# Performance work log

Measured on AMD Instinct MI355X. Metric: run time of the kernel, lower is better.

Reference implementation:

```python
import jax, jax.numpy as jnp
import numpy as np


def _gru_scan(x, m, d, Wih, Whh, bih, bhh):
    # Returns pre-update hidden at each step (hiddens.append(hidden) BEFORE rnn_cell)
    H = Whh.shape[1]
    B = x.shape[0]
    h0 = jnp.zeros((B, H), x.dtype)
    xs = (jnp.swapaxes(x, 0, 1), jnp.swapaxes(m, 0, 1), jnp.swapaxes(d, 0, 1))  # [T,B,V]

    def step(h, inp):
        xt, mt, dt = inp
        gi = jnp.concatenate([xt, mt, dt], axis=1) @ Wih.T + bih  # [B,3H]
        gh = h @ Whh.T + bhh
        ir, iz, inn = jnp.split(gi, 3, axis=1)
        hr, hz, hn = jnp.split(gh, 3, axis=1)
        r = jax.nn.sigmoid(ir + hr)
        z = jax.nn.sigmoid(iz + hz)
        n = jnp.tanh(inn + r * hn)
        h_new = (1.0 - z) * n + z * h
        return h_new, h

    _, hs = jax.lax.scan(step, h0, xs)
    return jnp.swapaxes(hs, 0, 1)  # [B,T,H]


def setup_inputs() -> dict:
    key = jax.random.key(0)
    B, T, V, H = 512, 128, 59, 512
    ks = jax.random.split(key, 12)

    def u(k, shape, fan_in):
        s = 1.0 / np.sqrt(fan_in).astype(np.float32)
        return jax.random.uniform(k, shape, jnp.float32, -s, s)

    return {
        "values": jax.random.normal(ks[0], (B, T, V), jnp.float32),
        "masks": (jax.random.uniform(ks[1], (B, T, V)) < 0.8).astype(jnp.float32),
        "deltas_f": jax.random.uniform(ks[2], (B, T, V), jnp.float32),
        "deltas_b": jax.random.uniform(ks[3], (B, T, V), jnp.float32),
        # GRUCell(input=3V, hidden=H)
        "Wih": u(ks[4], (3 * H, 3 * V), 3 * V),
        "Whh": u(ks[5], (3 * H, H), H),
        "bih": jnp.zeros((3 * H,), jnp.float32),
        "bhh": jnp.zeros((3 * H,), jnp.float32),
        # hist_reg: Linear(2H -> V)
        "Wh": u(ks[6], (V, 2 * H), 2 * H),
        "bh": jnp.zeros((V,), jnp.float32),
        "Wf": u(ks[7], (V, V), V),
        "bf": jnp.zeros((V,), jnp.float32),
        # weight_combine: Linear(2V -> V)
        "Wc": u(ks[8], (V, 2 * V), 2 * V),
        "bc": jnp.zeros((V,), jnp.float32),
        # imputation: Linear(V -> V)
        "Wi": u(ks[9], (V, V), V),
        "bi": jnp.zeros((V,), jnp.float32),
    }


def reference(values, masks, deltas_f, deltas_b, Wih, Whh, bih, bhh,
              Wh, bh, Wf, bf, Wc, bc, Wi, bi):
    V = values.shape[-1]
    # forward-direction hiddens
    hf = _gru_scan(values, masks, deltas_f, Wih, Whh, bih, bhh)  # [B,T,H]
    # backward-direction: run GRU on time-flipped x/masks with deltas_b, then reverse list
    hb = _gru_scan(values[:, ::-1], masks[:, ::-1], deltas_b, Wih, Whh, bih, bhh)[:, ::-1]
    h = jnp.concatenate([hf, hb], axis=-1)  # [B,T,2H]
    x_v = h @ Wh.T + bh  # hist_reg
    mdiag = 1.0 - jnp.eye(V, dtype=values.dtype)
    x_u = values @ (Wf * mdiag).T + bf  # feat_reg
    x_h = x_u + jnp.concatenate([x_v, masks], axis=-1) @ Wc.T + bc
    imp = x_h @ Wi.T + bi
    # per-timestep masked MAE, summed over T (denominator is per-step mask count)
    num = jnp.sum(jnp.abs(values - imp) * masks, axis=(0, 2))  # [T]
    den = jnp.sum(masks, axis=(0, 2)) + 1e-5
    x_loss = jnp.sum(num / den)
    x_imp = masks * values + (1.0 - masks) * imp
    return x_imp, x_loss
```

## Files before the change

### kernel.cpp

```cpp
#include <hip/hip_runtime.h>
#include <stdint.h>


typedef unsigned short ushort_t;
typedef __bf16 bf16x8 __attribute__((ext_vector_type(8)));
typedef float f32x4 __attribute__((ext_vector_type(4)));
typedef unsigned int u32x4 __attribute__((ext_vector_type(4)));

__device__ __forceinline__ ushort_t f2bf(float f) {
    union { float f; uint32_t u; } c; c.f = f;
    uint32_t u = c.u;
    uint32_t r = (u + 0x7FFFu + ((u >> 16) & 1u)) >> 16;
    return (ushort_t)r;
}

__device__ __forceinline__ u32x4 load_b128_cached(const void* p) {
    u32x4 d;
    asm volatile("global_load_dwordx4 %0, %1, off" : "=v"(d) : "v"(p) : "memory");
    return d;
}
__device__ __forceinline__ u32x4 load_b128_mall(const void* p) {
    u32x4 d;
    asm volatile("global_load_dwordx4 %0, %1, off sc0 sc1" : "=v"(d) : "v"(p) : "memory");
    return d;
}
__device__ __forceinline__ void store_b16_mall(void* p, unsigned v) {
    asm volatile("global_store_short %0, %1, off sc0 sc1" :: "v"(p), "v"(v) : "memory");
}

__device__ __forceinline__ float fast_sigmoid(float x) {
    float e = __expf(-x);
    return __builtin_amdgcn_rcpf(1.f + e);
}
__device__ __forceinline__ float fast_tanh(float x) {
    float xc = fminf(fmaxf(x, -15.f), 15.f);
    float e = __expf(-2.f * xc);
    return (1.f - e) * __builtin_amdgcn_rcpf(1.f + e);
}

__global__ void prep_small(const float* __restrict__ Wih, const float* __restrict__ Whh,
                           const float* __restrict__ Wh,
                           const float* __restrict__ Wf, const float* __restrict__ bf_,
                           const float* __restrict__ Wc, const float* __restrict__ bc,
                           const float* __restrict__ Wi, const float* __restrict__ bi,
                           ushort_t* __restrict__ WhhB, ushort_t* __restrict__ WihB,
                           ushort_t* __restrict__ WhpB,
                           ushort_t* __restrict__ hf0, ushort_t* __restrict__ hb0,
                           float* __restrict__ hstate,
                           ushort_t* __restrict__ Wpost1, ushort_t* __restrict__ Wpost2,
                           float* __restrict__ bcP, float* __restrict__ biP,
                           unsigned* __restrict__ bar, float* __restrict__ outp)
{
    long long gid = (long long)blockIdx.x * blockDim.x + threadIdx.x;
    long long stride = (long long)gridDim.x * blockDim.x;

    if (gid == 0) outp[3866624] = 0.f;
    for (long long i = gid; i < 16 * 64; i += stride) bar[i] = 0u;
    for (long long i = gid; i < 1024LL * 512; i += stride) hstate[i] = 0.f;
    for (long long i = gid; i < 512LL * 512; i += stride) { hf0[i] = 0; hb0[i] = 0; }
    for (long long i = gid; i < 1536LL * 512; i += stride) WhhB[i] = f2bf(Whh[i]);
    for (long long i = gid; i < 1536LL * 192; i += stride) {
        int n = (int)(i / 192), c = (int)(i % 192);
        WihB[i] = (c < 177) ? f2bf(Wih[n * 177 + c]) : (ushort_t)0;
    }
    for (long long i = gid; i < 64LL * 1024; i += stride) {
        int n = (int)(i >> 10), k = (int)(i & 1023);
        WhpB[i] = (n < 59) ? f2bf(Wh[n * 1024 + k]) : (ushort_t)0;
    }
    for (long long i = gid; i < 64LL * 192; i += stride) {
        int n = (int)(i / 192), c = (int)(i % 192);
        float w = 0.f;
        if (n < 59) {
            if (c < 59)       w = (c == n) ? 0.f : Wf[n * 59 + c];
            else if (c < 118) w = Wc[n * 118 + (c - 59)];
            else if (c < 177) w = Wc[n * 118 + 59 + (c - 118)];
        }
        Wpost1[i] = f2bf(w);
    }
    for (long long i = gid; i < 64LL * 64; i += stride) {
        int n = (int)(i >> 6), k = (int)(i & 63);
        Wpost2[i] = (n < 59 && k < 59) ? f2bf(Wi[n * 59 + k]) : (ushort_t)0;
    }
    for (long long i = gid; i < 64; i += stride) {
        bcP[i] = (i < 59) ? (bf_[i] + bc[i]) : 0.f;
        biP[i] = (i < 59) ? bi[i] : 0.f;
    }
}

__global__ __launch_bounds__(192)
void prep_panels(const float* __restrict__ values, const float* __restrict__ masks,
                 const float* __restrict__ deltas_f, const float* __restrict__ deltas_b,
                 ushort_t* __restrict__ xcat_f, ushort_t* __restrict__ xcat_b,
                 ushort_t* __restrict__ pcat)
{
    const int row = blockIdx.x;
    const int c = threadIdx.x;
    const int b = row >> 7, t = row & 127;
    const int tr = 127 - t;
    const long long rowr = (long long)b * 128 + tr;

    float vf = 0.f;
    if (c < 59)       vf = values  [(long long)row * 59 + c];
    else if (c < 118) vf = masks   [(long long)row * 59 + (c - 59)];
    else if (c < 177) vf = deltas_f[(long long)row * 59 + (c - 118)];
    xcat_f[((size_t)t * 512 + b) * 192 + c] = (c < 177) ? f2bf(vf) : (ushort_t)0;

    float vb = 0.f;
    if (c < 59)       vb = values  [rowr * 59 + c];
    else if (c < 118) vb = masks   [rowr * 59 + (c - 59)];
    else if (c < 177) vb = deltas_b[(long long)row * 59 + (c - 118)];
    xcat_b[((size_t)t * 512 + b) * 192 + c] = (c < 177) ? f2bf(vb) : (ushort_t)0;

    if (c < 59)
        pcat[(size_t)row * 192 + c] = f2bf(values[(long long)row * 59 + c]);
    else if (c >= 118 && c < 177)
        pcat[(size_t)row * 192 + c] = f2bf(masks[(long long)row * 59 + (c - 118)]);
    else if (c >= 177)
        pcat[(size_t)row * 192 + c] = 0;
}

__global__ __launch_bounds__(512)
void recurrence_kernel(const ushort_t* __restrict__ WhhB, const ushort_t* __restrict__ WihB,
                       const float* __restrict__ bih, const float* __restrict__ bhh,
                       const ushort_t* __restrict__ xcat_f, const ushort_t* __restrict__ xcat_b,
                       ushort_t* __restrict__ hfS, ushort_t* __restrict__ hbS,
                       unsigned* __restrict__ bar)
{
    extern __shared__ char smem_c[];
    ushort_t* Bw = (ushort_t*)smem_c;
    ushort_t* As = Bw + 96 * 704;

    const int tid  = threadIdx.x;
    const int blk  = blockIdx.x;
    const int ublk = blk & 15;
    const int mblk = blk >> 4;
    const int u0   = ublk * 32;
    const bool fwd = (mblk < 8);
    const int rbase = (fwd ? mblk : mblk - 8) * 64;
    const ushort_t* xbase = fwd ? xcat_f : xcat_b;
    ushort_t* hS = fwd ? hfS : hbS;
    unsigned* gctr = bar + (unsigned)mblk * 64;

    for (int i = tid; i < 96 * 88; i += 512) {
        int row = i / 88, q = i - row * 88;
        int g = row >> 5, u = u0 + (row & 31);
        const ushort_t* src = (q < 64)
            ? WhhB + ((size_t)(g * 512 + u)) * 512 + q * 8
            : WihB + ((size_t)(g * 512 + u)) * 192 + (q - 64) * 8;
        int qs = q ^ (row & 7);
        *(u32x4*)&Bw[row * 704 + qs * 8] = *(const u32x4*)src;
    }

    const int lane = tid & 63, wv = tid >> 6;
    const int mt = wv >> 1, tc = wv & 1;
    const int l15 = lane & 15, lhi = lane >> 4;
    const int arow = tid >> 3, aj = tid & 7;
    const int awoff = arow * 64 + ((aj ^ (arow & 7)) * 8);
    const int aSw = l15 & 7;

    const int u = u0 + tc * 16 + l15;
    const float bR  = bih[u] + bhh[u];
    const float bZ  = bih[512 + u] + bhh[512 + u];
    const float bNX = bih[1024 + u];
    const float bNH = bhh[1024 + u];
    asm volatile("" :: "v"(bR), "v"(bZ), "v"(bNX), "v"(bNH));
    asm volatile("s_waitcnt vmcnt(0) lgkmcnt(0)" ::: "memory");
    __syncthreads();

    f32x4 hreg = {0.f, 0.f, 0.f, 0.f};
    f32x4 zero = {0.f, 0.f, 0.f, 0.f};
    u32x4 rx[3];
    u32x4 rh[5];

    auto mfma_pos = [&](int cbuf, int jBbase, f32x4& aR, f32x4& aZ, f32x4& accN) {
        const ushort_t* Ab = As + cbuf * 4096;
        #pragma unroll
        for (int ks = 0; ks < 64; ks += 32) {
            int j  = (ks >> 3) + lhi;
            int jB = jBbase + j;
            bf16x8 a  = *(const bf16x8*)&Ab[(mt * 16 + l15) * 64 + ((j ^ aSw) * 8)];
            bf16x8 b0 = *(const bf16x8*)&Bw[( 0 + tc * 16 + l15) * 704 + ((jB ^ aSw) * 8)];
            bf16x8 b1 = *(const bf16x8*)&Bw[(32 + tc * 16 + l15) * 704 + ((jB ^ aSw) * 8)];
            bf16x8 b2 = *(const bf16x8*)&Bw[(64 + tc * 16 + l15) * 704 + ((jB ^ aSw) * 8)];
            aR   = __builtin_amdgcn_mfma_f32_16x16x32_bf16(a, b0, aR, 0, 0, 0);
            aZ   = __builtin_amdgcn_mfma_f32_16x16x32_bf16(a, b1, aZ, 0, 0, 0);
            accN = __builtin_amdgcn_mfma_f32_16x16x32_bf16(a, b2, accN, 0, 0, 0);
        }
    };

    {
        const ushort_t* xr0 = xbase + (size_t)(rbase + arow) * 192 + aj * 8;
        rx[0] = load_b128_cached(xr0);
        rx[1] = load_b128_cached(xr0 + 64);
        rx[2] = load_b128_cached(xr0 + 128);
    }
    asm volatile("s_waitcnt vmcnt(0)" ::: "memory");

    for (int t = 0; t < 127; ++t) {
        const ushort_t* hrow = hS + (size_t)t * 262144 + (size_t)(rbase + arow) * 512 + aj * 8;
        ushort_t* hdst = hS + (size_t)(t + 1) * 262144;

        f32x4 accR = zero, accZ = zero, accNX = zero, accNH = zero;

        rh[0] = load_b128_mall(hrow);
        rh[1] = load_b128_mall(hrow + 64);
        rh[2] = load_b128_mall(hrow + 128);

        *(u32x4*)&As[awoff] = rx[0];
        __syncthreads();

        mfma_pos(0, 64, accR, accZ, accNX);
        rh[3] = load_b128_mall(hrow + 3 * 64);
        *(u32x4*)&As[4096 + awoff] = rx[1];
        __syncthreads();

        mfma_pos(1, 72, accR, accZ, accNX);
        rh[4] = load_b128_mall(hrow + 4 * 64);
        *(u32x4*)&As[awoff] = rx[2];
        {
            const ushort_t* xrn = xbase + (size_t)(t + 1) * 98304
                                + (size_t)(rbase + arow) * 192 + aj * 8;
            rx[0] = load_b128_cached(xrn);
            rx[1] = load_b128_cached(xrn + 64);
            rx[2] = load_b128_cached(xrn + 128);
        }
        __syncthreads();

        mfma_pos(0, 80, accR, accZ, accNX);
        asm volatile("s_waitcnt vmcnt(7)" ::: "memory");
        *(u32x4*)&As[4096 + awoff] = rh[0];
        rh[0] = load_b128_mall(hrow + 5 * 64);
        __syncthreads();

        mfma_pos(1, 0, accR, accZ, accNH);
        asm volatile("s_waitcnt vmcnt(7)" ::: "memory");
        *(u32x4*)&As[awoff] = rh[1];
        rh[1] = load_b128_mall(hrow + 6 * 64);
        __syncthreads();

        mfma_pos(0, 8, accR, accZ, accNH);
        asm volatile("s_waitcnt vmcnt(7)" ::: "memory");
        *(u32x4*)&As[4096 + awoff] = rh[2];
        rh[2] = load_b128_mall(hrow + 7 * 64);
        __syncthreads();

        mfma_pos(1, 16, accR, accZ, accNH);
        asm volatile("s_waitcnt vmcnt(7)" ::: "memory");
        *(u32x4*)&As[awoff] = rh[3];
        __syncthreads();

        mfma_pos(0, 24, accR, accZ, accNH);
        asm volatile("s_waitcnt vmcnt(6)" ::: "memory");
        *(u32x4*)&As[4096 + awoff] = rh[4];
        __syncthreads();

        mfma_pos(1, 32, accR, accZ, accNH);
        asm volatile("s_waitcnt vmcnt(2)" ::: "memory");
        *(u32x4*)&As[awoff] = rh[0];
        __syncthreads();

        mfma_pos(0, 40, accR, accZ, accNH);
        asm volatile("s_waitcnt vmcnt(1)" ::: "memory");
        *(u32x4*)&As[4096 + awoff] = rh[1];
        __syncthreads();

        mfma_pos(1, 48, accR, accZ, accNH);
        asm volatile("s_waitcnt vmcnt(0)" ::: "memory");
        *(u32x4*)&As[awoff] = rh[2];
        __syncthreads();

        mfma_pos(0, 56, accR, accZ, accNH);

        #pragma unroll
        for (int reg = 0; reg < 4; ++reg) {
            int m = rbase + mt * 16 + lhi * 4 + reg;
            float rr = fast_sigmoid(accR[reg] + bR);
            float zz = fast_sigmoid(accZ[reg] + bZ);
            float nn = fast_tanh(accNX[reg] + bNX + rr * (accNH[reg] + bNH));
            float hnew = (1.f - zz) * nn + zz * hreg[reg];
            hreg[reg] = hnew;
            store_b16_mall(hdst + (size_t)m * 512 + u, (unsigned)f2bf(hnew));
        }

        if (t < 126) {
            asm volatile("s_waitcnt vmcnt(0)" ::: "memory");
            __syncthreads();
            if (tid == 0) {
                atomicAdd(gctr, 1u);
                unsigned target = (unsigned)(t + 1) * 16u;
                while (__hip_atomic_load(gctr, __ATOMIC_RELAXED,
                                         __HIP_MEMORY_SCOPE_AGENT) < target)
                    __builtin_amdgcn_s_sleep(1);
            }
            __syncthreads();
        }
    }
}

__global__ __launch_bounds__(512)
void step_kernel(const ushort_t* __restrict__ hsrcF, const ushort_t* __restrict__ hsrcB,
                 ushort_t* __restrict__ hdstF, ushort_t* __restrict__ hdstB,
                 const ushort_t* __restrict__ xF, const ushort_t* __restrict__ xB,
                 const ushort_t* __restrict__ WhhB, const ushort_t* __restrict__ WihB,
                 const float* __restrict__ bih, const float* __restrict__ bhh,
                 float* __restrict__ hstate)
{
    __shared__ __align__(16) ushort_t As[64 * 64];
    __shared__ __align__(16) ushort_t Bs[96 * 64];

    const int tid  = threadIdx.x;
    const int ublk = blockIdx.x;
    const int mblk = blockIdx.y;
    const int u0   = ublk * 32;
    const bool fwd = (mblk < 8);
    const ushort_t* hsrc = fwd ? hsrcF : hsrcB;
    const ushort_t* xsrc = fwd ? xF : xB;
    ushort_t* hdst = fwd ? hdstF : hdstB;
    const int rbase = (fwd ? mblk : mblk - 8) * 64;

    const int lane = tid & 63, wv = tid >> 6;
    const int mt = wv >> 1, tc = wv & 1;
    const int l15 = lane & 15, lhi = lane >> 4;

    f32x4 zero = {0.f, 0.f, 0.f, 0.f};
    f32x4 accR = zero, accZ = zero, accNH = zero, accNX = zero;
    const int arow = tid >> 3, ac8 = (tid & 7) * 8;

    for (int chunk = 0; chunk < 11; ++chunk) {
        const bool ph1 = (chunk < 8);
        {
            const ushort_t* src = ph1
                ? hsrc + ((size_t)(rbase + arow)) * 512 + chunk * 64 + ac8
                : xsrc + ((size_t)(rbase + arow)) * 192 + (chunk - 8) * 64 + ac8;
            *(uint4*)&As[arow * 64 + ac8] = *(const uint4*)src;
        }
        {
            int rowB = tid >> 3; int c8 = (tid & 7) * 8;
            int g = rowB >> 5; int u = u0 + (rowB & 31);
            const ushort_t* src = ph1
                ? WhhB + ((size_t)(g * 512 + u)) * 512 + chunk * 64 + c8
                : WihB + ((size_t)(g * 512 + u)) * 192 + (chunk - 8) * 64 + c8;
            *(uint4*)&Bs[rowB * 64 + c8] = *(const uint4*)src;
            if (tid < 256) {
                int u2 = tid + 512;
                rowB = u2 >> 3; c8 = (u2 & 7) * 8;
                g = rowB >> 5; u = u0 + (rowB & 31);
                src = ph1
                    ? WhhB + ((size_t)(g * 512 + u)) * 512 + chunk * 64 + c8
                    : WihB + ((size_t)(g * 512 + u)) * 192 + (chunk - 8) * 64 + c8;
                *(uint4*)&Bs[rowB * 64 + c8] = *(const uint4*)src;
            }
        }
        __syncthreads();
        #pragma unroll
        for (int ks = 0; ks < 64; ks += 32) {
            bf16x8 a  = *(const bf16x8*)&As[(mt * 16 + l15) * 64 + ks + lhi * 8];
            bf16x8 b0 = *(const bf16x8*)&Bs[( 0 + tc * 16 + l15) * 64 + ks + lhi * 8];
            bf16x8 b1 = *(const bf16x8*)&Bs[(32 + tc * 16 + l15) * 64 + ks + lhi * 8];
            bf16x8 b2 = *(const bf16x8*)&Bs[(64 + tc * 16 + l15) * 64 + ks + lhi * 8];
            accR = __builtin_amdgcn_mfma_f32_16x16x32_bf16(a, b0, accR, 0, 0, 0);
            accZ = __builtin_amdgcn_mfma_f32_16x16x32_bf16(a, b1, accZ, 0, 0, 0);
            if (ph1) accNH = __builtin_amdgcn_mfma_f32_16x16x32_bf16(a, b2, accNH, 0, 0, 0);
            else     accNX = __builtin_amdgcn_mfma_f32_16x16x32_bf16(a, b2, accNX, 0, 0, 0);
        }
        __syncthreads();
    }

    const int u = u0 + tc * 16 + l15;
    const float bR  = bih[u] + bhh[u];
    const float bZ  = bih[512 + u] + bhh[512 + u];
    const float bNX = bih[1024 + u];
    const float bNH = bhh[1024 + u];
    #pragma unroll
    for (int reg = 0; reg < 4; ++reg) {
        int m = mblk * 64 + mt * 16 + lhi * 4 + reg;
        float r = 1.f / (1.f + __expf(-(accR[reg] + bR)));
        float z = 1.f / (1.f + __expf(-(accZ[reg] + bZ)));
        float n = tanhf(accNX[reg] + bNX + r * (accNH[reg] + bNH));
        size_t idx = (size_t)m * 512 + u;
        float hold = hstate[idx];
        float hnew = (1.f - z) * n + z * hold;
        hstate[idx] = hnew;
        size_t bloc = (size_t)(fwd ? m : m - 512) * 512 + u;
        hdst[bloc] = f2bf(hnew);
    }
}

__global__ __launch_bounds__(256)
void xv_kernel(const ushort_t* __restrict__ hf, const ushort_t* __restrict__ hb,
               const ushort_t* __restrict__ WhpB, const float* __restrict__ bh,
               ushort_t* __restrict__ pcat)
{
    __shared__ __align__(16) ushort_t As[128 * 64];
    __shared__ __align__(16) ushort_t Bs[64 * 64];
    const int b = blockIdx.x;
    const int tid = threadIdx.x;
    const int lane = tid & 63, wv = tid >> 6;
    const int l15 = lane & 15, lhi = lane >> 4;

    f32x4 zero = {0.f, 0.f, 0.f, 0.f};
    f32x4 acc[2][4];
    #pragma unroll
    for (int i = 0; i < 2; ++i)
        #pragma unroll
        for (int j = 0; j < 4; ++j) acc[i][j] = zero;

    for (int chunk = 0; chunk < 16; ++chunk) {
        const bool fw = (chunk < 8);
        #pragma unroll
        for (int s = 0; s < 4; ++s) {
            int unit = tid + s * 256;
            int row = unit >> 3;
            int c8 = (unit & 7) * 8;
            const ushort_t* src = fw
                ? hf + ((size_t)row * 512 + b) * 512 + chunk * 64 + c8
                : hb + ((size_t)(127 - row) * 512 + b) * 512 + (chunk - 8) * 64 + c8;
            *(uint4*)&As[row * 64 + c8] = *(const uint4*)src;
        }
        #pragma unroll
        for (int s = 0; s < 2; ++s) {
            int unit = tid + s * 256;
            int row = unit >> 3;
            int c8 = (unit & 7) * 8;
            *(uint4*)&Bs[row * 64 + c8] =
                *(const uint4*)(WhpB + (size_t)row * 1024 + chunk * 64 + c8);
        }
        __syncthreads();
        #pragma unroll
        for (int ks = 0; ks < 64; ks += 32) {
            bf16x8 bfr[4];
            #pragma unroll
            for (int nt = 0; nt < 4; ++nt)
                bfr[nt] = *(const bf16x8*)&Bs[(nt * 16 + l15) * 64 + ks + lhi * 8];
            #pragma unroll
            for (int mt2 = 0; mt2 < 2; ++mt2) {
                bf16x8 a = *(const bf16x8*)&As[(wv * 32 + mt2 * 16 + l15) * 64 + ks + lhi * 8];
                #pragma unroll
                for (int nt = 0; nt < 4; ++nt)
                    acc[mt2][nt] = __builtin_amdgcn_mfma_f32_16x16x32_bf16(a, bfr[nt], acc[mt2][nt], 0, 0, 0);
            }
        }
        __syncthreads();
    }
    #pragma unroll
    for (int mt2 = 0; mt2 < 2; ++mt2) {
        #pragma unroll
        for (int nt = 0; nt < 4; ++nt) {
            int col = nt * 16 + l15;
            if (col < 59) {
                float bhc = bh[col];
                #pragma unroll
                for (int reg = 0; reg < 4; ++reg) {
                    int t = wv * 32 + mt2 * 16 + lhi * 4 + reg;
                    pcat[((size_t)b * 128 + t) * 192 + 59 + col] = f2bf(acc[mt2][nt][reg] + bhc);
                }
            }
        }
    }
}

__global__ __launch_bounds__(256)
void post_kernel(const ushort_t* __restrict__ pcat,
                 const ushort_t* __restrict__ Wpost1, const ushort_t* __restrict__ Wpost2,
                 const float* __restrict__ bcP, const float* __restrict__ biP,
                 const float* __restrict__ values, const float* __restrict__ masks,
                 float* __restrict__ out, float* __restrict__ pnum, float* __restrict__ pden)
{
    __shared__ __align__(16) ushort_t A1[64 * 200];
    __shared__ __align__(16) ushort_t B1[64 * 200];
    __shared__ __align__(16) ushort_t B2[64 * 72];

    const int tid = threadIdx.x;
    const int blk = blockIdx.x;
    const int lane = tid & 63, wv = tid >> 6;
    const int l15 = lane & 15, lhi = lane >> 4;

    #pragma unroll
    for (int s = 0; s < 6; ++s) {
        int unit = tid + s * 256;
        int row = unit / 24, c8 = (unit % 24) * 8;
        *(uint4*)&A1[row * 200 + c8] =
            *(const uint4*)(pcat + ((size_t)blk * 64 + row) * 192 + c8);
        *(uint4*)&B1[row * 200 + c8] =
            *(const uint4*)(Wpost1 + (size_t)row * 192 + c8);
    }
    #pragma unroll
    for (int s = 0; s < 2; ++s) {
        int unit = tid + s * 256;
        int row = unit >> 3, c8 = (unit & 7) * 8;
        *(uint4*)&B2[row * 72 + c8] = *(const uint4*)(Wpost2 + (size_t)row * 64 + c8);
    }
    __syncthreads();

    f32x4 zero = {0.f, 0.f, 0.f, 0.f};
    f32x4 acc1[4];
    #pragma unroll
    for (int nt = 0; nt < 4; ++nt) acc1[nt] = zero;

    #pragma unroll
// ... 52 lines not shown
                dsum += m;
            }
        }
        #pragma unroll
        for (int o = 1; o < 16; o <<= 1) {
            esum += __shfl_xor(esum, o);
            dsum += __shfl_xor(dsum, o);
        }
        if (l15 == 0) { pnum[rowg] = esum; pden[rowg] = dsum; }
    }
}

__global__ __launch_bounds__(256)
void loss_kernel(const float* __restrict__ pnum, const float* __restrict__ pden,
                 float* __restrict__ out)
{
    __shared__ float sn[4], sd[4];
    const int t = blockIdx.x;
    const int tid = threadIdx.x;
    float a = 0.f, b = 0.f;
    for (int bb = tid; bb < 512; bb += 256) {
        a += pnum[(size_t)bb * 128 + t];
        b += pden[(size_t)bb * 128 + t];
    }
    #pragma unroll
    for (int o = 32; o >= 1; o >>= 1) {
        a += __shfl_xor(a, o);
        b += __shfl_xor(b, o);
    }
    const int wv = tid >> 6;
    if ((tid & 63) == 0) { sn[wv] = a; sd[wv] = b; }
    __syncthreads();
    if (tid == 0) {
        float A = sn[0] + sn[1] + sn[2] + sn[3];
        float B = sd[0] + sd[1] + sd[2] + sd[3];
        atomicAdd(out + 3866624, A / (B + 1e-5f));
    }
}

extern "C" void kernel_launch(void* const* d_in, const int* in_sizes, int n_in,
                              void* d_out, int out_size, void* d_ws, size_t ws_size,
                              hipStream_t stream)
{
    const float* values   = (const float*)d_in[0];
    const float* masks    = (const float*)d_in[1];
    const float* deltas_f = (const float*)d_in[2];
    const float* deltas_b = (const float*)d_in[3];
    const float* Wih = (const float*)d_in[4];
    const float* Whh = (const float*)d_in[5];
    const float* bih = (const float*)d_in[6];
    const float* bhh = (const float*)d_in[7];
    const float* Wh  = (const float*)d_in[8];
    const float* bh  = (const float*)d_in[9];
    const float* Wf  = (const float*)d_in[10];
    const float* bf_ = (const float*)d_in[11];
    const float* Wc  = (const float*)d_in[12];
    const float* bc  = (const float*)d_in[13];
    const float* Wi  = (const float*)d_in[14];
    const float* bi  = (const float*)d_in[15];
    float* out = (float*)d_out;

    uint8_t* ws = (uint8_t*)d_ws;
    size_t off = 0;
    auto alloc = [&](size_t bytes) -> void* {
        void* p = ws + off;
        off = (off + bytes + 255) & ~((size_t)255);
        return p;
    };
    ushort_t* xcat_f = (ushort_t*)alloc(128ULL * 512 * 192 * 2);
    ushort_t* xcat_b = (ushort_t*)alloc(128ULL * 512 * 192 * 2);
    ushort_t* WhhB   = (ushort_t*)alloc(1536ULL * 512 * 2);
    ushort_t* WihB   = (ushort_t*)alloc(1536ULL * 192 * 2);
    ushort_t* WhpB   = (ushort_t*)alloc(64ULL * 1024 * 2);
    ushort_t* hfS    = (ushort_t*)alloc(128ULL * 512 * 512 * 2);
    ushort_t* hbS    = (ushort_t*)alloc(128ULL * 512 * 512 * 2);
    float*    hstate = (float*)alloc(1024ULL * 512 * 4);
    ushort_t* pcat   = (ushort_t*)alloc(65536ULL * 192 * 2);
    ushort_t* Wpost1 = (ushort_t*)alloc(64ULL * 192 * 2);
    ushort_t* Wpost2 = (ushort_t*)alloc(64ULL * 64 * 2);
    float*    bcP    = (float*)alloc(64 * 4);
    float*    biP    = (float*)alloc(64 * 4);
    float*    pnum   = (float*)alloc(65536ULL * 4);
    float*    pden   = (float*)alloc(65536ULL * 4);
    unsigned* bar    = (unsigned*)alloc(16 * 64 * 4);

    prep_small<<<1024, 256, 0, stream>>>(Wih, Whh, Wh, Wf, bf_, Wc, bc, Wi, bi,
                                         WhhB, WihB, WhpB, hfS, hbS, hstate,
                                         Wpost1, Wpost2, bcP, biP, bar, out);
    prep_panels<<<65536, 192, 0, stream>>>(values, masks, deltas_f, deltas_b,
                                           xcat_f, xcat_b, pcat);

    const unsigned smemBytes = (96u * 704u + 2u * 64u * 64u) * 2u;
    hipError_t aerr = hipFuncSetAttribute((const void*)recurrence_kernel,
                                          hipFuncAttributeMaxDynamicSharedMemorySize,
                                          (int)smemBytes);
    hipError_t lerr = hipErrorUnknown;
    if (aerr == hipSuccess) {
        const ushort_t* a0 = WhhB; const ushort_t* a1 = WihB;
        const float* a2 = bih; const float* a3 = bhh;
        const ushort_t* a4 = xcat_f; const ushort_t* a5 = xcat_b;
        ushort_t* a6 = hfS; ushort_t* a7 = hbS;
        unsigned* a8 = bar;
        void* args[] = { &a0, &a1, &a2, &a3, &a4, &a5, &a6, &a7, &a8 };
        lerr = hipLaunchCooperativeKernel((const void*)recurrence_kernel,
                                          dim3(256), dim3(512), args, smemBytes, stream);
    }
    if (lerr != hipSuccess) {
        for (int t = 0; t < 127; ++t) {
            step_kernel<<<dim3(16, 16), 512, 0, stream>>>(
                hfS + (size_t)t * 512 * 512, hbS + (size_t)t * 512 * 512,
                hfS + (size_t)(t + 1) * 512 * 512, hbS + (size_t)(t + 1) * 512 * 512,
                xcat_f + (size_t)t * 512 * 192, xcat_b + (size_t)t * 512 * 192,
                WhhB, WihB, bih, bhh, hstate);
        }
    }

    xv_kernel<<<512, 256, 0, stream>>>(hfS, hbS, WhpB, bh, pcat);
    post_kernel<<<1024, 256, 0, stream>>>(pcat, Wpost1, Wpost2, bcP, biP,
                                          values, masks, out, pnum, pden);
    loss_kernel<<<128, 256, 0, stream>>>(pnum, pden, out);
}
```

Baseline: 840.4 us.

## Replace global atomic barrier with per-producer flags and slab-blocked hidden layout

The hidden-state buffer is re-laid out so that each 32-unit column block is a contiguous slab. Each block can then write its outputs with coalesced 8-byte stores staged through LDS, instead of scattered 2-byte stores. The single atomic counter barrier per row group is replaced by per-producer flag words. Consumers poll only the 8 producers whose slab they are about to read, and split that wait so the second half overlaps the input-projection MFMAs. Block-to-(row,unit) mapping is also permuted, and h loads now use L2-scoped hints, with stores written to both L2 and MALL. This risks subtle memory-ordering issues between the flag stores and the data stores, and the layout change requires matching updates in the fallback and xv kernels.

```diff
diff --git a/kernel.cpp b/kernel.cpp
--- a/kernel.cpp
+++ b/kernel.cpp
@@ -6,6 +6,7 @@
 typedef __bf16 bf16x8 __attribute__((ext_vector_type(8)));
 typedef float f32x4 __attribute__((ext_vector_type(4)));
 typedef unsigned int u32x4 __attribute__((ext_vector_type(4)));
+typedef unsigned int u32x2 __attribute__((ext_vector_type(2)));
 
 __device__ __forceinline__ ushort_t f2bf(float f) {
     union { float f; uint32_t u; } c; c.f = f;
@@ -19,13 +20,19 @@
     asm volatile("global_load_dwordx4 %0, %1, off" : "=v"(d) : "v"(p) : "memory");
     return d;
 }
-__device__ __forceinline__ u32x4 load_b128_mall(const void* p) {
+__device__ __forceinline__ u32x4 load_b128_l2(const void* p) {
     u32x4 d;
-    asm volatile("global_load_dwordx4 %0, %1, off sc0 sc1" : "=v"(d) : "v"(p) : "memory");
+    asm volatile("global_load_dwordx4 %0, %1, off sc0" : "=v"(d) : "v"(p) : "memory");
     return d;
 }
-__device__ __forceinline__ void store_b16_mall(void* p, unsigned v) {
-    asm volatile("global_store_short %0, %1, off sc0 sc1" :: "v"(p), "v"(v) : "memory");
+__device__ __forceinline__ void store_b64_l2(void* p, u32x2 v) {
+    asm volatile("global_store_dwordx2 %0, %1, off sc0" :: "v"(p), "v"(v) : "memory");
+}
+__device__ __forceinline__ void store_b64_mall(void* p, u32x2 v) {
+    asm volatile("global_store_dwordx2 %0, %1, off sc0 sc1" :: "v"(p), "v"(v) : "memory");
+}
+__device__ __forceinline__ void store_u32_mall(void* p, unsigned v) {
+    asm volatile("global_store_dword %0, %1, off sc0 sc1" :: "v"(p), "v"(v) : "memory");
 }
 
 __device__ __forceinline__ float fast_sigmoid(float x) {
@@ -132,8 +139,8 @@
 
     const int tid  = threadIdx.x;
     const int blk  = blockIdx.x;
-    const int ublk = blk & 15;
-    const int mblk = blk >> 4;
+    const int ublk = blk >> 4;
+    const int mblk = ((blk & 7) << 1) | ((blk >> 3) & 1);
     const int u0   = ublk * 32;
     const bool fwd = (mblk < 8);
     const int rbase = (fwd ? mblk : mblk - 8) * 64;
@@ -170,7 +177,7 @@
     f32x4 hreg = {0.f, 0.f, 0.f, 0.f};
     f32x4 zero = {0.f, 0.f, 0.f, 0.f};
     u32x4 rx[3];
-    u32x4 rh[5];
+    u32x4 rh[8];
 
     auto mfma_pos = [&](int cbuf, int jBbase, f32x4& aR, f32x4& aZ, f32x4& accN) {
         const ushort_t* Ab = As + cbuf * 4096;
@@ -188,6 +195,9 @@
         }
     };
 
+    const size_t hoff = (size_t)(aj >> 2) * 16384
+                      + (size_t)(rbase + arow) * 32 + (size_t)(aj & 3) * 8;
+
     {
         const ushort_t* xr0 = xbase + (size_t)(rbase + arow) * 192 + aj * 8;
         rx[0] = load_b128_cached(xr0);
@@ -197,25 +207,60 @@
     asm volatile("s_waitcnt vmcnt(0)" ::: "memory");
 
     for (int t = 0; t < 127; ++t) {
-        const ushort_t* hrow = hS + (size_t)t * 262144 + (size_t)(rbase + arow) * 512 + aj * 8;
+        const ushort_t* hslab = hS + (size_t)t * 262144;
         ushort_t* hdst = hS + (size_t)(t + 1) * 262144;
 
         f32x4 accR = zero, accZ = zero, accNX = zero, accNH = zero;
 
-        rh[0] = load_b128_mall(hrow);
-        rh[1] = load_b128_mall(hrow + 64);
-        rh[2] = load_b128_mall(hrow + 128);
+        if (t > 0) {
+            if (wv == 0) {
+                bool part = (lane < 8) && (lane != ublk);
+                const unsigned* ap = gctr + lane;
+                for (;;) {
+                    bool ok = true;
+                    if (part) {
+                        unsigned v;
+                        asm volatile("global_load_dword %0, %1, off sc0 sc1\n\t"
+                                     "s_waitcnt vmcnt(0)"
+                                     : "=v"(v) : "v"(ap) : "memory");
+                        ok = (v >= (unsigned)t);
+                    }
+                    if (__ballot(ok) == ~0ULL) break;
+                    __builtin_amdgcn_s_sleep(1);
+                }
+            }
+            __syncthreads();
+        }
+
+        rh[0] = load_b128_l2(hslab + hoff);
+        rh[1] = load_b128_l2(hslab + hoff + 32768);
+        rh[2] = load_b128_l2(hslab + hoff + 2 * 32768);
+        rh[3] = load_b128_l2(hslab + hoff + 3 * 32768);
 
         *(u32x4*)&As[awoff] = rx[0];
         __syncthreads();
 
         mfma_pos(0, 64, accR, accZ, accNX);
-        rh[3] = load_b128_mall(hrow + 3 * 64);
         *(u32x4*)&As[4096 + awoff] = rx[1];
         __syncthreads();
 
         mfma_pos(1, 72, accR, accZ, accNX);
-        rh[4] = load_b128_mall(hrow + 4 * 64);
+        if (t > 0 && wv == 0) {
+            bool part = (lane >= 8) && (lane < 16) && (lane != ublk);
+            const unsigned* ap = gctr + lane;
+            for (;;) {
+                bool ok = true;
+                if (part) {
+                    unsigned v;
+                    asm volatile("global_load_dword %0, %1, off sc0 sc1\n\t"
+                                 "s_waitcnt vmcnt(4)"
+                                 : "=v"(v) : "v"(ap) : "memory");
+                    ok = (v >= (unsigned)t);
+                }
+                if (__ballot(ok) == ~0ULL) break;
+                __builtin_amdgcn_s_sleep(1);
+            }
+        }
         *(u32x4*)&As[awoff] = rx[2];
         {
             const ushort_t* xrn = xbase + (size_t)(t + 1) * 98304
@@ -227,21 +272,22 @@
         __syncthreads();
 
         mfma_pos(0, 80, accR, accZ, accNX);
-        asm volatile("s_waitcnt vmcnt(7)" ::: "memory");
+        rh[4] = load_b128_l2(hslab + hoff + 4 * 32768);
+        rh[5] = load_b128_l2(hslab + hoff + 5 * 32768);
+        rh[6] = load_b128_l2(hslab + hoff + 6 * 32768);
+        rh[7] = load_b128_l2(hslab + hoff + 7 * 32768);
+        asm volatile("s_waitcnt vmcnt(10)" ::: "memory");
         *(u32x4*)&As[4096 + awoff] = rh[0];
-        rh[0] = load_b128_mall(hrow + 5 * 64);
         __syncthreads();
 
         mfma_pos(1, 0, accR, accZ, accNH);
-        asm volatile("s_waitcnt vmcnt(7)" ::: "memory");
+        asm volatile("s_waitcnt vmcnt(9)" ::: "memory");
         *(u32x4*)&As[awoff] = rh[1];
-        rh[1] = load_b128_mall(hrow + 6 * 64);
         __syncthreads();
 
         mfma_pos(0, 8, accR, accZ, accNH);
-        asm volatile("s_waitcnt vmcnt(7)" ::: "memory");
+        asm volatile("s_waitcnt vmcnt(8)" ::: "memory");
         *(u32x4*)&As[4096 + awoff] = rh[2];
-        rh[2] = load_b128_mall(hrow + 7 * 64);
         __syncthreads();
 
         mfma_pos(1, 16, accR, accZ, accNH);
@@ -250,50 +296,52 @@
         __syncthreads();
 
         mfma_pos(0, 24, accR, accZ, accNH);
-        asm volatile("s_waitcnt vmcnt(6)" ::: "memory");
+        asm volatile("s_waitcnt vmcnt(3)" ::: "memory");
         *(u32x4*)&As[4096 + awoff] = rh[4];
         __syncthreads();
 
         mfma_pos(1, 32, accR, accZ, accNH);
         asm volatile("s_waitcnt vmcnt(2)" ::: "memory");
-        *(u32x4*)&As[awoff] = rh[0];
+        *(u32x4*)&As[awoff] = rh[5];
         __syncthreads();
 
         mfma_pos(0, 40, accR, accZ, accNH);
         asm volatile("s_waitcnt vmcnt(1)" ::: "memory");
-        *(u32x4*)&As[4096 + awoff] = rh[1];
+        *(u32x4*)&As[4096 + awoff] = rh[6];
         __syncthreads();
 
         mfma_pos(1, 48, accR, accZ, accNH);
         asm volatile("s_waitcnt vmcnt(0)" ::: "memory");
-        *(u32x4*)&As[awoff] = rh[2];
+        *(u32x4*)&As[awoff] = rh[7];
         __syncthreads();
 
         mfma_pos(0, 56, accR, accZ, accNH);
 
         #pragma unroll
         for (int reg = 0; reg < 4; ++reg) {
-            int m = rbase + mt * 16 + lhi * 4 + reg;
+            int r64 = mt * 16 + lhi * 4 + reg;
             float rr = fast_sigmoid(accR[reg] + bR);
             float zz = fast_sigmoid(accZ[reg] + bZ);
             float nn = fast_tanh(accNX[reg] + bNX + rr * (accNH[reg] + bNH));
             float hnew = (1.f - zz) * nn + zz * hreg[reg];
             hreg[reg] = hnew;
-            store_b16_mall(hdst + (size_t)m * 512 + u, (unsigned)f2bf(hnew));
-        }
-
-        if (t < 126) {
-            asm volatile("s_waitcnt vmcnt(0)" ::: "memory");
-            __syncthreads();
-            if (tid == 0) {
-                atomicAdd(gctr, 1u);
-                unsigned target = (unsigned)(t + 1) * 16u;
-                while (__hip_atomic_load(gctr, __ATOMIC_RELAXED,
-                                         __HIP_MEMORY_SCOPE_AGENT) < target)
-                    __builtin_amdgcn_s_sleep(1);
-            }
-            __syncthreads();
-        }
+            As[4096 + r64 * 40 + (tc * 16 + l15)] = f2bf(hnew);
+        }
+        __syncthreads();
+        {
+            int r64 = tid >> 3;
+            int c4  = (tid & 7) * 4;
+            u32x2 v = *(const u32x2*)&As[4096 + r64 * 40 + c4];
+            ushort_t* dst = hdst + (size_t)ublk * 16384
+                          + (size_t)(rbase + r64) * 32 + c4;
+            store_b64_l2(dst, v);
+            store_b64_mall(dst, v);
+        }
+        asm volatile("s_waitcnt vmcnt(0)" ::: "memory");
+        __syncthreads();
+
+        if (t < 126 && tid == 0)
+            store_u32_mall(gctr + ublk, (unsigned)(t + 1));
     }
 }
 
@@ -329,9 +377,13 @@
     for (int chunk = 0; chunk < 11; ++chunk) {
         const bool ph1 = (chunk < 8);
         {
-            const ushort_t* src = ph1
-                ? hsrc + ((size_t)(rbase + arow)) * 512 + chunk * 64 + ac8
-                : xsrc + ((size_t)(rbase + arow)) * 192 + (chunk - 8) * 64 + ac8;
+            const ushort_t* src;
+            if (ph1) {
+                int p = 2 * chunk + (ac8 >> 5);
+                src = hsrc + (size_t)p * 16384 + (size_t)(rbase + arow) * 32 + (ac8 & 31);
+            } else {
+                src = xsrc + ((size_t)(rbase + arow)) * 192 + (chunk - 8) * 64 + ac8;
+            }
             *(uint4*)&As[arow * 64 + ac8] = *(const uint4*)src;
         }
         {
@@ -381,7 +433,8 @@
         float hold = hstate[idx];
         float hnew = (1.f - z) * n + z * hold;
         hstate[idx] = hnew;
-        size_t bloc = (size_t)(fwd ? m : m - 512) * 512 + u;
+        int ml = fwd ? m : m - 512;
+        size_t bloc = (size_t)(u >> 5) * 16384 + (size_t)ml * 32 + (u & 31);
         hdst[bloc] = f2bf(hnew);
     }
 }
@@ -412,9 +465,13 @@
             int unit = tid + s * 256;
             int row = unit >> 3;
             int c8 = (unit & 7) * 8;
-            const ushort_t* src = fw
-                ? hf + ((size_t)row * 512 + b) * 512 + chunk * 64 + c8
-                : hb + ((size_t)(127 - row) * 512 + b) * 512 + (chunk - 8) * 64 + c8;
+            int ch = fw ? chunk : (chunk - 8);
+            int col = ch * 64 + c8;
+            int p = col >> 5, cc = col & 31;
+            int ti = fw ? row : (127 - row);
+            const ushort_t* hbase = fw ? hf : hb;
+            const ushort_t* src = hbase + (size_t)ti * 262144
+                                + (size_t)p * 16384 + (size_t)b * 32 + cc;
             *(uint4*)&As[row * 64 + c8] = *(const uint4*)src;
         }
         #pragma unroll
```

Result: slower. 998.0 us (+18.8%).

## Replace block-wide barrier with per-wave flag polling and direct register A-fragments

Applied to the files above, without the earlier changes.

Each wave now loads its own h and x A-fragments straight from global memory into registers, so the LDS staging buffer and the many __syncthreads per timestep are gone. The per-block atomic counter barrier is replaced by per-wave slot flags: each wave publishes its step number to its own padded slot and polls the 32 slots of the waves sharing its 16-row band. The aim is to cut global synchronization latency and intra-block barriers on the serial critical path. In exchange it uses more global loads per wave and relies on the cache-scope modifiers to keep cross-block visibility correct.

```diff
diff --git a/kernel.cpp b/kernel.cpp
--- a/kernel.cpp
+++ b/kernel.cpp
@@ -19,13 +19,19 @@
     asm volatile("global_load_dwordx4 %0, %1, off" : "=v"(d) : "v"(p) : "memory");
     return d;
 }
-__device__ __forceinline__ u32x4 load_b128_mall(const void* p) {
+__device__ __forceinline__ u32x4 load_b128_l2(const void* p) {
     u32x4 d;
-    asm volatile("global_load_dwordx4 %0, %1, off sc0 sc1" : "=v"(d) : "v"(p) : "memory");
+    asm volatile("global_load_dwordx4 %0, %1, off sc0" : "=v"(d) : "v"(p) : "memory");
     return d;
+}
+__device__ __forceinline__ void store_b16_l2(void* p, unsigned v) {
+    asm volatile("global_store_short %0, %1, off sc0" :: "v"(p), "v"(v) : "memory");
 }
 __device__ __forceinline__ void store_b16_mall(void* p, unsigned v) {
     asm volatile("global_store_short %0, %1, off sc0 sc1" :: "v"(p), "v"(v) : "memory");
+}
+__device__ __forceinline__ void store_u32_mall(void* p, unsigned v) {
+    asm volatile("global_store_dword %0, %1, off sc0 sc1" :: "v"(p), "v"(v) : "memory");
 }
 
 __device__ __forceinline__ float fast_sigmoid(float x) {
@@ -55,7 +61,7 @@
     long long stride = (long long)gridDim.x * blockDim.x;
 
     if (gid == 0) outp[3866624] = 0.f;
-    for (long long i = gid; i < 16 * 64; i += stride) bar[i] = 0u;
+    for (long long i = gid; i < 2048LL * 16; i += stride) bar[i] = 0u;
     for (long long i = gid; i < 1024LL * 512; i += stride) hstate[i] = 0.f;
     for (long long i = gid; i < 512LL * 512; i += stride) { hf0[i] = 0; hb0[i] = 0; }
     for (long long i = gid; i < 1536LL * 512; i += stride) WhhB[i] = f2bf(Whh[i]);
@@ -128,7 +134,6 @@
 {
     extern __shared__ char smem_c[];
     ushort_t* Bw = (ushort_t*)smem_c;
-    ushort_t* As = Bw + 96 * 704;
 
     const int tid  = threadIdx.x;
     const int blk  = blockIdx.x;
@@ -139,7 +144,6 @@
     const int rbase = (fwd ? mblk : mblk - 8) * 64;
     const ushort_t* xbase = fwd ? xcat_f : xcat_b;
     ushort_t* hS = fwd ? hfS : hbS;
-    unsigned* gctr = bar + (unsigned)mblk * 64;
 
     for (int i = tid; i < 96 * 88; i += 512) {
         int row = i / 88, q = i - row * 88;
@@ -154,8 +158,6 @@
     const int lane = tid & 63, wv = tid >> 6;
     const int mt = wv >> 1, tc = wv & 1;
     const int l15 = lane & 15, lhi = lane >> 4;
-    const int arow = tid >> 3, aj = tid & 7;
-    const int awoff = arow * 64 + ((aj ^ (arow & 7)) * 8);
     const int aSw = l15 & 7;
 
     const int u = u0 + tc * 16 + l15;
@@ -167,134 +169,127 @@
     asm volatile("s_waitcnt vmcnt(0) lgkmcnt(0)" ::: "memory");
     __syncthreads();
 
+    const unsigned bandSlot = (unsigned)(mblk * 4 + mt) * 32u;
+    const unsigned* pollp = bar + ((size_t)bandSlot + (unsigned)lane) * 16;
+    unsigned* myslot = bar + ((size_t)bandSlot + (unsigned)(ublk * 2 + tc)) * 16;
+
     f32x4 hreg = {0.f, 0.f, 0.f, 0.f};
     f32x4 zero = {0.f, 0.f, 0.f, 0.f};
-    u32x4 rx[3];
-    u32x4 rh[5];
-
-    auto mfma_pos = [&](int cbuf, int jBbase, f32x4& aR, f32x4& aZ, f32x4& accN) {
-        const ushort_t* Ab = As + cbuf * 4096;
-        #pragma unroll
-        for (int ks = 0; ks < 64; ks += 32) {
-            int j  = (ks >> 3) + lhi;
-            int jB = jBbase + j;
-            bf16x8 a  = *(const bf16x8*)&Ab[(mt * 16 + l15) * 64 + ((j ^ aSw) * 8)];
+    f32x4 accR, accZ, accNX, accNH;
+
+    u32x4 h0a, h0b, h1a, h1b, h2a, h2b, h3a, h3b;
+    u32x4 h4a, h4b, h5a, h5b, h6a, h6b, h7a, h7b;
+    u32x4 rx0a, rx0b, rx1a, rx1b, rx2a, rx2b;
+
+    auto mfma6 = [&](u32x4 fa, u32x4 fb, int jb, f32x4& accN) {
+        bf16x8 a0 = *(bf16x8*)&fa;
+        bf16x8 a1 = *(bf16x8*)&fb;
+        {
+            int jB = jb + lhi;
             bf16x8 b0 = *(const bf16x8*)&Bw[( 0 + tc * 16 + l15) * 704 + ((jB ^ aSw) * 8)];
             bf16x8 b1 = *(const bf16x8*)&Bw[(32 + tc * 16 + l15) * 704 + ((jB ^ aSw) * 8)];
             bf16x8 b2 = *(const bf16x8*)&Bw[(64 + tc * 16 + l15) * 704 + ((jB ^ aSw) * 8)];
-            aR   = __builtin_amdgcn_mfma_f32_16x16x32_bf16(a, b0, aR, 0, 0, 0);
-            aZ   = __builtin_amdgcn_mfma_f32_16x16x32_bf16(a, b1, aZ, 0, 0, 0);
-            accN = __builtin_amdgcn_mfma_f32_16x16x32_bf16(a, b2, accN, 0, 0, 0);
+            accR = __builtin_amdgcn_mfma_f32_16x16x32_bf16(a0, b0, accR, 0, 0, 0);
+            accZ = __builtin_amdgcn_mfma_f32_16x16x32_bf16(a0, b1, accZ, 0, 0, 0);
+            accN = __builtin_amdgcn_mfma_f32_16x16x32_bf16(a0, b2, accN, 0, 0, 0);
+        }
+        {
+            int jB = jb + 4 + lhi;
+            bf16x8 b0 = *(const bf16x8*)&Bw[( 0 + tc * 16 + l15) * 704 + ((jB ^ aSw) * 8)];
+            bf16x8 b1 = *(const bf16x8*)&Bw[(32 + tc * 16 + l15) * 704 + ((jB ^ aSw) * 8)];
+            bf16x8 b2 = *(const bf16x8*)&Bw[(64 + tc * 16 + l15) * 704 + ((jB ^ aSw) * 8)];
+            accR = __builtin_amdgcn_mfma_f32_16x16x32_bf16(a1, b0, accR, 0, 0, 0);
+            accZ = __builtin_amdgcn_mfma_f32_16x16x32_bf16(a1, b1, accZ, 0, 0, 0);
+            accN = __builtin_amdgcn_mfma_f32_16x16x32_bf16(a1, b2, accN, 0, 0, 0);
         }
     };
 
+    const size_t mrow = (size_t)(rbase + mt * 16 + l15);
+
     {
-        const ushort_t* xr0 = xbase + (size_t)(rbase + arow) * 192 + aj * 8;
-        rx[0] = load_b128_cached(xr0);
-        rx[1] = load_b128_cached(xr0 + 64);
-        rx[2] = load_b128_cached(xr0 + 128);
+        const ushort_t* xr = xbase + (mrow) * 192 + lhi * 8;
+        rx0a = load_b128_cached(xr);        rx0b = load_b128_cached(xr + 32);
+        rx1a = load_b128_cached(xr + 64);   rx1b = load_b128_cached(xr + 96);
+        rx2a = load_b128_cached(xr + 128);  rx2b = load_b128_cached(xr + 160);
     }
     asm volatile("s_waitcnt vmcnt(0)" ::: "memory");
+    __builtin_amdgcn_sched_barrier(0);
+
+#define HPOS(K, WN, JB)                                                       \
+    asm volatile("s_waitcnt vmcnt(" #WN ")" ::: "memory");                    \
+    __builtin_amdgcn_sched_barrier(0);                                        \
+    mfma6(h##K##a, h##K##b, (JB), accNH);
 
     for (int t = 0; t < 127; ++t) {
-        const ushort_t* hrow = hS + (size_t)t * 262144 + (size_t)(rbase + arow) * 512 + aj * 8;
-        ushort_t* hdst = hS + (size_t)(t + 1) * 262144;
-
-        f32x4 accR = zero, accZ = zero, accNX = zero, accNH = zero;
-
-        rh[0] = load_b128_mall(hrow);
-        rh[1] = load_b128_mall(hrow + 64);
-        rh[2] = load_b128_mall(hrow + 128);
-
-        *(u32x4*)&As[awoff] = rx[0];
-        __syncthreads();
-
-        mfma_pos(0, 64, accR, accZ, accNX);
-        rh[3] = load_b128_mall(hrow + 3 * 64);
-        *(u32x4*)&As[4096 + awoff] = rx[1];
-        __syncthreads();
-
-        mfma_pos(1, 72, accR, accZ, accNX);
-        rh[4] = load_b128_mall(hrow + 4 * 64);
-        *(u32x4*)&As[awoff] = rx[2];
+        if (t > 0) {
+            const unsigned target = (unsigned)t;
+            for (;;) {
+                unsigned v = 0xFFFFFFFFu;
+                if (lane < 32) {
+                    asm volatile("global_load_dword %0, %1, off sc0 sc1"
+                                 : "=v"(v) : "v"(pollp) : "memory");
+                }
+                asm volatile("s_waitcnt vmcnt(0)" ::: "memory");
+                if (__ballot(v >= target) == ~0ULL) break;
+                __builtin_amdgcn_s_sleep(1);
+            }
+            __builtin_amdgcn_sched_barrier(0);
+        }
+
         {
-            const ushort_t* xrn = xbase + (size_t)(t + 1) * 98304
-                                + (size_t)(rbase + arow) * 192 + aj * 8;
-            rx[0] = load_b128_cached(xrn);
-            rx[1] = load_b128_cached(xrn + 64);
-            rx[2] = load_b128_cached(xrn + 128);
-        }
-        __syncthreads();
-
-        mfma_pos(0, 80, accR, accZ, accNX);
-        asm volatile("s_waitcnt vmcnt(7)" ::: "memory");
-        *(u32x4*)&As[4096 + awoff] = rh[0];
-        rh[0] = load_b128_mall(hrow + 5 * 64);
-        __syncthreads();
-
-        mfma_pos(1, 0, accR, accZ, accNH);
-        asm volatile("s_waitcnt vmcnt(7)" ::: "memory");
-        *(u32x4*)&As[awoff] = rh[1];
-        rh[1] = load_b128_mall(hrow + 6 * 64);
-        __syncthreads();
-
-        mfma_pos(0, 8, accR, accZ, accNH);
-        asm volatile("s_waitcnt vmcnt(7)" ::: "memory");
-        *(u32x4*)&As[4096 + awoff] = rh[2];
-        rh[2] = load_b128_mall(hrow + 7 * 64);
-        __syncthreads();
-
-        mfma_pos(1, 16, accR, accZ, accNH);
-        asm volatile("s_waitcnt vmcnt(7)" ::: "memory");
-        *(u32x4*)&As[awoff] = rh[3];
-        __syncthreads();
-
-        mfma_pos(0, 24, accR, accZ, accNH);
-        asm volatile("s_waitcnt vmcnt(6)" ::: "memory");
-        *(u32x4*)&As[4096 + awoff] = rh[4];
-        __syncthreads();
-
-        mfma_pos(1, 32, accR, accZ, accNH);
-        asm volatile("s_waitcnt vmcnt(2)" ::: "memory");
-        *(u32x4*)&As[awoff] = rh[0];
-        __syncthreads();
-
-        mfma_pos(0, 40, accR, accZ, accNH);
-        asm volatile("s_waitcnt vmcnt(1)" ::: "memory");
-        *(u32x4*)&As[4096 + awoff] = rh[1];
-        __syncthreads();
-
-        mfma_pos(1, 48, accR, accZ, accNH);
+            const ushort_t* hr = hS + (size_t)t * 262144 + mrow * 512 + lhi * 8;
+            h0a = load_b128_l2(hr);            h0b = load_b128_l2(hr + 32);
+            h1a = load_b128_l2(hr + 64);       h1b = load_b128_l2(hr + 96);
+            h2a = load_b128_l2(hr + 128);      h2b = load_b128_l2(hr + 160);
+            h3a = load_b128_l2(hr + 192);      h3b = load_b128_l2(hr + 224);
+            h4a = load_b128_l2(hr + 256);      h4b = load_b128_l2(hr + 288);
+            h5a = load_b128_l2(hr + 320);      h5b = load_b128_l2(hr + 352);
+            h6a = load_b128_l2(hr + 384);      h6b = load_b128_l2(hr + 416);
+            h7a = load_b128_l2(hr + 448);      h7b = load_b128_l2(hr + 480);
+        }
+
+        accR = zero; accZ = zero; accNX = zero; accNH = zero;
+        mfma6(rx0a, rx0b, 64, accNX);
+        mfma6(rx1a, rx1b, 72, accNX);
+        mfma6(rx2a, rx2b, 80, accNX);
+
+        {
+            const ushort_t* xr = xbase + ((size_t)(t + 1) * 512 + mrow) * 192 + lhi * 8;
+            rx0a = load_b128_cached(xr);        rx0b = load_b128_cached(xr + 32);
+            rx1a = load_b128_cached(xr + 64);   rx1b = load_b128_cached(xr + 96);
+            rx2a = load_b128_cached(xr + 128);  rx2b = load_b128_cached(xr + 160);
+        }
+
+        HPOS(0, 20,  0)
+        HPOS(1, 18,  8)
+        HPOS(2, 16, 16)
+        HPOS(3, 14, 24)
+        HPOS(4, 12, 32)
+        HPOS(5, 10, 40)
+        HPOS(6,  8, 48)
+        HPOS(7,  6, 56)
+
+        {
+            ushort_t* hdst = hS + (size_t)(t + 1) * 262144;
+            #pragma unroll
+            for (int reg = 0; reg < 4; ++reg) {
+                float rr = fast_sigmoid(accR[reg] + bR);
+                float zz = fast_sigmoid(accZ[reg] + bZ);
+                float nn = fast_tanh(accNX[reg] + bNX + rr * (accNH[reg] + bNH));
+                float hnew = (1.f - zz) * nn + zz * hreg[reg];
+                hreg[reg] = hnew;
+                unsigned hb16 = (unsigned)f2bf(hnew);
+                ushort_t* dst = hdst + (size_t)(rbase + mt * 16 + lhi * 4 + reg) * 512 + u;
+                store_b16_l2(dst, hb16);
+                store_b16_mall(dst, hb16);
+            }
+        }
         asm volatile("s_waitcnt vmcnt(0)" ::: "memory");
-        *(u32x4*)&As[awoff] = rh[2];
-        __syncthreads();
-
-        mfma_pos(0, 56, accR, accZ, accNH);
-
-        #pragma unroll
-        for (int reg = 0; reg < 4; ++reg) {
-            int m = rbase + mt * 16 + lhi * 4 + reg;
-            float rr = fast_sigmoid(accR[reg] + bR);
-            float zz = fast_sigmoid(accZ[reg] + bZ);
-            float nn = fast_tanh(accNX[reg] + bNX + rr * (accNH[reg] + bNH));
-            float hnew = (1.f - zz) * nn + zz * hreg[reg];
-            hreg[reg] = hnew;
-            store_b16_mall(hdst + (size_t)m * 512 + u, (unsigned)f2bf(hnew));
-        }
-
-        if (t < 126) {
-            asm volatile("s_waitcnt vmcnt(0)" ::: "memory");
-            __syncthreads();
-            if (tid == 0) {
-                atomicAdd(gctr, 1u);
-                unsigned target = (unsigned)(t + 1) * 16u;
-                while (__hip_atomic_load(gctr, __ATOMIC_RELAXED,
-                                         __HIP_MEMORY_SCOPE_AGENT) < target)
-                    __builtin_amdgcn_s_sleep(1);
-            }
-            __syncthreads();
-        }
-    }
+
+        if (lane == 0)
+            store_u32_mall(myslot, (unsigned)(t + 1));
+    }
+#undef HPOS
 }
 
 __global__ __launch_bounds__(512)
@@ -633,7 +628,7 @@
     float*    biP    = (float*)alloc(64 * 4);
     float*    pnum   = (float*)alloc(65536ULL * 4);
     float*    pden   = (float*)alloc(65536ULL * 4);
-    unsigned* bar    = (unsigned*)alloc(16 * 64 * 4);
+    unsigned* bar    = (unsigned*)alloc(2048ULL * 16 * 4);
 
     prep_small<<<1024, 256, 0, stream>>>(Wih, Whh, Wh, Wf, bf_, Wc, bc, Wi, bi,
                                          WhhB, WihB, WhpB, hfS, hbS, hstate,
@@ -641,7 +636,7 @@
     prep_panels<<<65536, 192, 0, stream>>>(values, masks, deltas_f, deltas_b,
                                            xcat_f, xcat_b, pcat);
 
-    const unsigned smemBytes = (96u * 704u + 2u * 64u * 64u) * 2u;
+    const unsigned smemBytes = 96u * 704u * 2u;
     hipError_t aerr = hipFuncSetAttribute((const void*)recurrence_kernel,
                                           hipFuncAttributeMaxDynamicSharedMemorySize,
                                           (int)smemBytes);
```

Measured after the change: 3.112 ms. +270.3%, slower.

## Store hidden state in column-slab layout and remap blocks for L2 locality

Applied to the files above, without the earlier changes.

Changes the per-timestep hidden-state buffer from row-major [B,512] to 16 column slabs of [512,32], so each block writes a contiguous slab. Block-to-tile mapping is permuted so blocks sharing a unit slice are adjacent, and h loads switch from MALL-scope to L2-scope (sc0). Each store is issued twice, once at L2 scope and once at MALL scope, to keep cross-XCD visibility. All consumers (fallback recurrence, xv_kernel) are updated to the new indexing. The duplicated store and the weaker load scope could cause coherence problems across XCDs.

```diff
diff --git a/kernel.cpp b/kernel.cpp
--- a/kernel.cpp
+++ b/kernel.cpp
@@ -19,10 +19,13 @@
     asm volatile("global_load_dwordx4 %0, %1, off" : "=v"(d) : "v"(p) : "memory");
     return d;
 }
-__device__ __forceinline__ u32x4 load_b128_mall(const void* p) {
+__device__ __forceinline__ u32x4 load_b128_l2(const void* p) {
     u32x4 d;
-    asm volatile("global_load_dwordx4 %0, %1, off sc0 sc1" : "=v"(d) : "v"(p) : "memory");
+    asm volatile("global_load_dwordx4 %0, %1, off sc0" : "=v"(d) : "v"(p) : "memory");
     return d;
+}
+__device__ __forceinline__ void store_b16_l2(void* p, unsigned v) {
+    asm volatile("global_store_short %0, %1, off sc0" :: "v"(p), "v"(v) : "memory");
 }
 __device__ __forceinline__ void store_b16_mall(void* p, unsigned v) {
     asm volatile("global_store_short %0, %1, off sc0 sc1" :: "v"(p), "v"(v) : "memory");
@@ -132,8 +135,8 @@
 
     const int tid  = threadIdx.x;
     const int blk  = blockIdx.x;
-    const int ublk = blk & 15;
-    const int mblk = blk >> 4;
+    const int ublk = blk >> 4;
+    const int mblk = ((blk & 7) << 1) | ((blk >> 3) & 1);
     const int u0   = ublk * 32;
     const bool fwd = (mblk < 8);
     const int rbase = (fwd ? mblk : mblk - 8) * 64;
@@ -159,6 +162,7 @@
     const int aSw = l15 & 7;
 
     const int u = u0 + tc * 16 + l15;
+    const int cl = tc * 16 + l15;
     const float bR  = bih[u] + bhh[u];
     const float bZ  = bih[512 + u] + bhh[512 + u];
     const float bNX = bih[1024 + u];
@@ -188,6 +192,9 @@
         }
     };
 
+    const size_t hoff = (size_t)(aj >> 2) * 16384
+                      + (size_t)(rbase + arow) * 32 + (size_t)(aj & 3) * 8;
+
     {
         const ushort_t* xr0 = xbase + (size_t)(rbase + arow) * 192 + aj * 8;
         rx[0] = load_b128_cached(xr0);
@@ -197,25 +204,25 @@
     asm volatile("s_waitcnt vmcnt(0)" ::: "memory");
 
     for (int t = 0; t < 127; ++t) {
-        const ushort_t* hrow = hS + (size_t)t * 262144 + (size_t)(rbase + arow) * 512 + aj * 8;
+        const ushort_t* hslab = hS + (size_t)t * 262144 + hoff;
         ushort_t* hdst = hS + (size_t)(t + 1) * 262144;
 
         f32x4 accR = zero, accZ = zero, accNX = zero, accNH = zero;
 
-        rh[0] = load_b128_mall(hrow);
-        rh[1] = load_b128_mall(hrow + 64);
-        rh[2] = load_b128_mall(hrow + 128);
+        rh[0] = load_b128_l2(hslab);
+        rh[1] = load_b128_l2(hslab + 32768);
+        rh[2] = load_b128_l2(hslab + 2 * 32768);
 
         *(u32x4*)&As[awoff] = rx[0];
         __syncthreads();
 
         mfma_pos(0, 64, accR, accZ, accNX);
-        rh[3] = load_b128_mall(hrow + 3 * 64);
+        rh[3] = load_b128_l2(hslab + 3 * 32768);
         *(u32x4*)&As[4096 + awoff] = rx[1];
         __syncthreads();
 
         mfma_pos(1, 72, accR, accZ, accNX);
-        rh[4] = load_b128_mall(hrow + 4 * 64);
+        rh[4] = load_b128_l2(hslab + 4 * 32768);
         *(u32x4*)&As[awoff] = rx[2];
         {
             const ushort_t* xrn = xbase + (size_t)(t + 1) * 98304
@@ -229,19 +236,19 @@
         mfma_pos(0, 80, accR, accZ, accNX);
         asm volatile("s_waitcnt vmcnt(7)" ::: "memory");
         *(u32x4*)&As[4096 + awoff] = rh[0];
-        rh[0] = load_b128_mall(hrow + 5 * 64);
+        rh[0] = load_b128_l2(hslab + 5 * 32768);
         __syncthreads();
 
         mfma_pos(1, 0, accR, accZ, accNH);
         asm volatile("s_waitcnt vmcnt(7)" ::: "memory");
         *(u32x4*)&As[awoff] = rh[1];
-        rh[1] = load_b128_mall(hrow + 6 * 64);
+        rh[1] = load_b128_l2(hslab + 6 * 32768);
         __syncthreads();
 
         mfma_pos(0, 8, accR, accZ, accNH);
         asm volatile("s_waitcnt vmcnt(7)" ::: "memory");
         *(u32x4*)&As[4096 + awoff] = rh[2];
-        rh[2] = load_b128_mall(hrow + 7 * 64);
+        rh[2] = load_b128_l2(hslab + 7 * 32768);
         __syncthreads();
 
         mfma_pos(1, 16, accR, accZ, accNH);
@@ -279,7 +286,10 @@
             float nn = fast_tanh(accNX[reg] + bNX + rr * (accNH[reg] + bNH));
             float hnew = (1.f - zz) * nn + zz * hreg[reg];
             hreg[reg] = hnew;
-            store_b16_mall(hdst + (size_t)m * 512 + u, (unsigned)f2bf(hnew));
+            unsigned hb16 = (unsigned)f2bf(hnew);
+            ushort_t* dst = hdst + (size_t)ublk * 16384 + (size_t)m * 32 + cl;
+            store_b16_l2(dst, hb16);
+            store_b16_mall(dst, hb16);
         }
 
         if (t < 126) {
@@ -329,9 +339,13 @@
     for (int chunk = 0; chunk < 11; ++chunk) {
         const bool ph1 = (chunk < 8);
         {
-            const ushort_t* src = ph1
-                ? hsrc + ((size_t)(rbase + arow)) * 512 + chunk * 64 + ac8
-                : xsrc + ((size_t)(rbase + arow)) * 192 + (chunk - 8) * 64 + ac8;
+            const ushort_t* src;
+            if (ph1) {
+                int p = 2 * chunk + (ac8 >> 5);
+                src = hsrc + (size_t)p * 16384 + (size_t)(rbase + arow) * 32 + (ac8 & 31);
+            } else {
+                src = xsrc + ((size_t)(rbase + arow)) * 192 + (chunk - 8) * 64 + ac8;
+            }
             *(uint4*)&As[arow * 64 + ac8] = *(const uint4*)src;
         }
         {
@@ -381,7 +395,8 @@
         float hold = hstate[idx];
         float hnew = (1.f - z) * n + z * hold;
         hstate[idx] = hnew;
-        size_t bloc = (size_t)(fwd ? m : m - 512) * 512 + u;
+        int ml = fwd ? m : m - 512;
+        size_t bloc = (size_t)(u >> 5) * 16384 + (size_t)ml * 32 + (u & 31);
         hdst[bloc] = f2bf(hnew);
     }
 }
@@ -412,9 +427,13 @@
             int unit = tid + s * 256;
             int row = unit >> 3;
             int c8 = (unit & 7) * 8;
-            const ushort_t* src = fw
-                ? hf + ((size_t)row * 512 + b) * 512 + chunk * 64 + c8
-                : hb + ((size_t)(127 - row) * 512 + b) * 512 + (chunk - 8) * 64 + c8;
+            int ch = fw ? chunk : (chunk - 8);
+            int col = ch * 64 + c8;
+            int p = col >> 5, cc = col & 31;
+            int ti = fw ? row : (127 - row);
+            const ushort_t* hbase = fw ? hf : hb;
+            const ushort_t* src = hbase + (size_t)ti * 262144
+                                + (size_t)p * 16384 + (size_t)b * 32 + cc;
             *(uint4*)&As[row * 64 + c8] = *(const uint4*)src;
         }
         #pragma unroll
```

New measurement: 2.935 ms. +249.2%, slower.
